# Kernel optimization log

Hardware: AMD Instinct MI355X
Metric: run time of the kernel (lower is better)

The kernel has to match this reference:

```python
import jax, jax.numpy as jnp
import numpy as np

B, T, I = 64, 256, 768   # batch, seq_len (sentences), input_dim
H = 384                  # hidden per direction (hidden_dim // 2)
D = 768                  # hidden_dim (bidirectional concat)


def _gru_dir(x_tbi, w_ih, w_hh, b_ih, b_hh, reverse):
    """Single-direction GRU, PyTorch gate order [r, z, n]. x_tbi: [T,B,in]."""
    gx = jnp.einsum('tbi,gi->tbg', x_tbi, w_ih) + b_ih  # [T,B,3H] input gates

    def step(h, g):
        gh = h @ w_hh.T + b_hh                       # [B,3H]
        r = jax.nn.sigmoid(g[..., :H] + gh[..., :H])
        z = jax.nn.sigmoid(g[..., H:2 * H] + gh[..., H:2 * H])
        n = jnp.tanh(g[..., 2 * H:] + r * gh[..., 2 * H:])
        h_new = (1.0 - z) * n + z * h
        return h_new, h_new

    h0 = jnp.zeros((x_tbi.shape[1], H), x_tbi.dtype)
    _, ys = jax.lax.scan(step, h0, gx, reverse=reverse)  # ys in time order
    return ys


def setup_inputs() -> dict:
    key = jax.random.key(0)
    ks = jax.random.split(key, 24)
    s = 0.05
    inp = {"Sentences": jax.random.normal(ks[0], (B, T, I), dtype=jnp.float32)}
    idx = 1
    for l, in_dim in ((0, I), (1, D)):
        for d in ("f", "b"):
            inp[f"w_ih_l{l}{d}"] = jax.random.normal(ks[idx], (3 * H, in_dim), dtype=jnp.float32) * s; idx += 1
            inp[f"w_hh_l{l}{d}"] = jax.random.normal(ks[idx], (3 * H, H), dtype=jnp.float32) * s; idx += 1
            inp[f"b_ih_l{l}{d}"] = jax.random.normal(ks[idx], (3 * H,), dtype=jnp.float32) * s; idx += 1
            inp[f"b_hh_l{l}{d}"] = jax.random.normal(ks[idx], (3 * H,), dtype=jnp.float32) * s; idx += 1
    inp["fc_w"] = jax.random.normal(ks[idx], (D, D), dtype=jnp.float32) * s; idx += 1
    inp["fc_b"] = jax.random.normal(ks[idx], (D,), dtype=jnp.float32) * s; idx += 1
    inp["upw_w"] = jax.random.normal(ks[idx], (1, D), dtype=jnp.float32) * s; idx += 1
    inp["upw_b"] = jax.random.normal(ks[idx], (1,), dtype=jnp.float32) * s
    return inp


def reference(Sentences,
              w_ih_l0f, w_hh_l0f, b_ih_l0f, b_hh_l0f,
              w_ih_l0b, w_hh_l0b, b_ih_l0b, b_hh_l0b,
              w_ih_l1f, w_hh_l1f, b_ih_l1f, b_hh_l1f,
              w_ih_l1b, w_hh_l1b, b_ih_l1b, b_hh_l1b,
              fc_w, fc_b, upw_w, upw_b):
    x = jnp.transpose(Sentences, (1, 0, 2))  # [T,B,I]
    # layer 0, bidirectional
    hf = _gru_dir(x, w_ih_l0f, w_hh_l0f, b_ih_l0f, b_hh_l0f, reverse=False)
    hb = _gru_dir(x, w_ih_l0b, w_hh_l0b, b_ih_l0b, b_hh_l0b, reverse=True)
    x = jnp.concatenate([hf, hb], axis=-1)  # [T,B,D]
    # layer 1, bidirectional
    hf = _gru_dir(x, w_ih_l1f, w_hh_l1f, b_ih_l1f, b_hh_l1f, reverse=False)
    hb = _gru_dir(x, w_ih_l1b, w_hh_l1b, b_ih_l1b, b_hh_l1b, reverse=True)
    hidden = jnp.transpose(jnp.concatenate([hf, hb], axis=-1), (1, 0, 2))  # [B,T,D]
    # additive attention pooling
    u = jnp.tanh(hidden @ fc_w.T + fc_b)            # [B,T,D]
    logits = u @ upw_w.T + upw_b                    # [B,T,1]
    alpha = jax.nn.softmax(logits, axis=1)          # softmax over sentences
    return jnp.sum(alpha * hidden, axis=-2)         # [B,D]
```

## Files before the change

kernel.cpp:

```cpp
#include <hip/hip_runtime.h>

#define BB   64
#define TT   256
#define II   768
#define HH   384
#define DD   768
#define G3   1152
#define G6   2304

#define TILE 128
#define BK   16

typedef unsigned long long u64t;
typedef __attribute__((ext_vector_type(4))) unsigned int u32x4;

__global__ __launch_bounds__(256) void gemm_gx(
    const float* __restrict__ X, int xmode,
    const float* __restrict__ wf, const float* __restrict__ wb,
    const float* __restrict__ bif, const float* __restrict__ bib,
    float* __restrict__ gx)
{
    __shared__ float As[BK][TILE + 4];
    __shared__ float Bs[BK][TILE + 4];
    const int tid = threadIdx.x;
    const int tx = tid & 15, ty = tid >> 4;
    const int m0 = blockIdx.y * TILE;
    const int n0 = blockIdx.x * TILE;

    float acc[8][8];
#pragma unroll
    for (int i = 0; i < 8; i++)
#pragma unroll
        for (int j = 0; j < 8; j++) acc[i][j] = 0.f;

    for (int k0 = 0; k0 < 768; k0 += BK) {
#pragma unroll
        for (int l = 0; l < 2; l++) {
            int id = tid + l * 256;
            int r  = id >> 2;
            int kq = (id & 3) * 4;
            int m  = m0 + r;
            const float* src;
            if (xmode == 0) {
                int b = m & 63, t = m >> 6;
                src = X + (size_t)b * (TT * II) + (size_t)t * II + k0 + kq;
            } else {
                src = X + (size_t)m * 768 + k0 + kq;
            }
            float4 v = *(const float4*)src;
            As[kq + 0][r] = v.x; As[kq + 1][r] = v.y;
            As[kq + 2][r] = v.z; As[kq + 3][r] = v.w;
        }
#pragma unroll
        for (int l = 0; l < 2; l++) {
            int id = tid + l * 256;
            int r  = id >> 2;
            int kq = (id & 3) * 4;
            int n  = n0 + r;
            const float* wsrc = (n < G3) ? (wf + (size_t)n * 768)
                                         : (wb + (size_t)(n - G3) * 768);
            float4 v = *(const float4*)(wsrc + k0 + kq);
            Bs[kq + 0][r] = v.x; Bs[kq + 1][r] = v.y;
            Bs[kq + 2][r] = v.z; Bs[kq + 3][r] = v.w;
        }
        __syncthreads();
#pragma unroll
        for (int kk = 0; kk < BK; ++kk) {
            float av[8], bv[8];
            *(float4*)&av[0] = *(const float4*)&As[kk][ty * 8];
            *(float4*)&av[4] = *(const float4*)&As[kk][ty * 8 + 4];
            *(float4*)&bv[0] = *(const float4*)&Bs[kk][tx * 8];
            *(float4*)&bv[4] = *(const float4*)&Bs[kk][tx * 8 + 4];
#pragma unroll
            for (int i = 0; i < 8; i++)
#pragma unroll
                for (int j = 0; j < 8; j++)
                    acc[i][j] = fmaf(av[i], bv[j], acc[i][j]);
        }
        __syncthreads();
    }

#pragma unroll
    for (int i = 0; i < 8; i++) {
        int m = m0 + ty * 8 + i;
        int t = m >> 6, b = m & 63;
        float* dst = gx + ((size_t)t * G6 + n0 + tx * 8) * 64 + b;
#pragma unroll
        for (int j = 0; j < 8; j++) {
            int n = n0 + tx * 8 + j;
            float bias = (n < G3) ? bif[n] : bib[n - G3];
            dst[(size_t)j * 64] = acc[i][j] + bias;
        }
    }
}

__global__ __launch_bounds__(256) void recur5(
    const float* __restrict__ gxT,
    const float* __restrict__ whf, const float* __restrict__ whb,
    const float* __restrict__ bhf, const float* __restrict__ bhb,
    u64t* __restrict__ hbuf,
    float* __restrict__ out)
{
    __shared__ float part[2][4][12][64];

    const int bid  = blockIdx.x;
    const int dir  = bid / 96;
    const int c0   = (bid % 96) * 4;
    const int tid  = threadIdx.x;
    const int lane = tid & 63;
    const int w    = __builtin_amdgcn_readfirstlane(tid >> 6);
    const int c    = c0 + w;

    const float* wh = dir ? whb : whf;
    const float* bh = dir ? bhb : bhf;

    const float* wpp[12];
#pragma unroll
    for (int cc = 0; cc < 4; cc++)
#pragma unroll
        for (int g = 0; g < 3; g++)
            wpp[cc * 3 + g] = wh + (size_t)(g * HH + c0 + cc) * HH + w * 96;

    const float bhr = bh[c], bhz = bh[HH + c], bhn = bh[2 * HH + c];

    u64t* hb = hbuf + (size_t)dir * 2 * (192 * 64 * 2);
    const unsigned va0 = (unsigned)(lane * 16);
    const unsigned va1 = va0 + 4096;
    const unsigned va2 = va0 + 8192;

    float hprev = 0.f;

    for (int s = 0; s < TT; s++) {
        const int t = dir ? (TT - 1 - s) : s;
        const u64t* hcur = hb + (size_t)(s & 1) * (192 * 64 * 2);
        u64t*       hnxt = hb + (size_t)((s & 1) ^ 1) * (192 * 64 * 2);
        const unsigned want = (unsigned)s;

        const float* g0 = gxT + ((size_t)t * G6 + dir * G3) * 64;
        float gr = g0[(size_t)(0 * HH + c) * 64 + lane];
        float gz = g0[(size_t)(1 * HH + c) * 64 + lane];
        float gn = g0[(size_t)(2 * HH + c) * 64 + lane];

        float acc[12];
#pragma unroll
        for (int i = 0; i < 12; i++) acc[i] = 0.f;

#pragma unroll 1
        for (int blk = 0; blk < 4; blk++) {
            const u64t* bp = hcur + (size_t)(w * 48 + blk * 12) * 128;
            unsigned long long base = (unsigned long long)bp;
            u32x4 r[12];

            while (true) {
                asm volatile(
                    "global_load_dwordx4 %0, %12, %15 sc0 sc1\n\t"
                    "global_load_dwordx4 %1, %12, %15 offset:1024 sc0 sc1\n\t"
                    "global_load_dwordx4 %2, %12, %15 offset:2048 sc0 sc1\n\t"
                    "global_load_dwordx4 %3, %12, %15 offset:3072 sc0 sc1\n\t"
                    "global_load_dwordx4 %4, %13, %15 sc0 sc1\n\t"
                    "global_load_dwordx4 %5, %13, %15 offset:1024 sc0 sc1\n\t"
                    "global_load_dwordx4 %6, %13, %15 offset:2048 sc0 sc1\n\t"
                    "global_load_dwordx4 %7, %13, %15 offset:3072 sc0 sc1\n\t"
                    "global_load_dwordx4 %8, %14, %15 sc0 sc1\n\t"
                    "global_load_dwordx4 %9, %14, %15 offset:1024 sc0 sc1\n\t"
                    "global_load_dwordx4 %10, %14, %15 offset:2048 sc0 sc1\n\t"
                    "global_load_dwordx4 %11, %14, %15 offset:3072 sc0 sc1\n\t"
                    "s_waitcnt vmcnt(0)"
                    : "=&v"(r[0]), "=&v"(r[1]), "=&v"(r[2]), "=&v"(r[3]),
                      "=&v"(r[4]), "=&v"(r[5]), "=&v"(r[6]), "=&v"(r[7]),
                      "=&v"(r[8]), "=&v"(r[9]), "=&v"(r[10]), "=&v"(r[11])
                    : "v"(va0), "v"(va1), "v"(va2), "s"(base)
                    : "memory");

                bool ok = true;
#pragma unroll
                for (int jj = 0; jj < 12; jj++)
                    ok = ok && (r[jj].y == want) && (r[jj].w == want);
                if (__all(ok)) break;
                __builtin_amdgcn_s_sleep(1);
            }

#pragma unroll
            for (int jj = 0; jj < 12; jj++) {
                float v0 = __uint_as_float(r[jj].x);
                float v1 = __uint_as_float(r[jj].z);
                const int ko = blk * 24 + jj * 2;
#pragma unroll
                for (int cg = 0; cg < 12; cg++) {
                    acc[cg] = fmaf(v0, wpp[cg][ko],     acc[cg]);
                    acc[cg] = fmaf(v1, wpp[cg][ko + 1], acc[cg]);
                }
            }
        }

#pragma unroll
        for (int cg = 0; cg < 12; cg++)
            part[s & 1][w][cg][lane] = acc[cg];
        __syncthreads();

        const int d0 = w * 3;
        float ar = part[s & 1][0][d0 + 0][lane] + part[s & 1][1][d0 + 0][lane]
                 + part[s & 1][2][d0 + 0][lane] + part[s & 1][3][d0 + 0][lane];
        float az = part[s & 1][0][d0 + 1][lane] + part[s & 1][1][d0 + 1][lane]
                 + part[s & 1][2][d0 + 1][lane] + part[s & 1][3][d0 + 1][lane];
        float an = part[s & 1][0][d0 + 2][lane] + part[s & 1][1][d0 + 2][lane]
                 + part[s & 1][2][d0 + 2][lane] + part[s & 1][3][d0 + 2][lane];

        float ghr = ar + bhr, ghz = az + bhz, ghn = an + bhn;
        float rr  = 1.f / (1.f + expf(-(gr + ghr)));
        float zz  = 1.f / (1.f + expf(-(gz + ghz)));
        float nn  = tanhf(gn + rr * ghn);
        float hnew = (1.f - zz) * nn + zz * hprev;
        hprev = hnew;

        u64t pv = ((u64t)(unsigned)(s + 1) << 32) | (u64t)__float_as_uint(hnew);
        __hip_atomic_store(hnxt + (size_t)(c >> 1) * 128 + lane * 2 + (c & 1),
                           pv, __ATOMIC_RELAXED, __HIP_MEMORY_SCOPE_AGENT);
        out[(size_t)t * (BB * DD) + (size_t)lane * DD + dir * HH + c] = hnew;
    }
}

__global__ __launch_bounds__(256) void attn_logits(
    const float* __restrict__ Xh,
    const float* __restrict__ fcw,
    const float* __restrict__ fcb, const float* __restrict__ upw,
    float* __restrict__ logits)
{
    __shared__ float As[BK][TILE + 4];
    __shared__ float Bs[BK][TILE + 4];
    __shared__ float red[TILE][17];
    const int tid = threadIdx.x;
    const int tx = tid & 15, ty = tid >> 4;
    const int m0 = blockIdx.y * TILE;
    const int n0 = blockIdx.x * TILE;

    float acc[8][8];
#pragma unroll
    for (int i = 0; i < 8; i++)
#pragma unroll
        for (int j = 0; j < 8; j++) acc[i][j] = 0.f;

    for (int k0 = 0; k0 < 768; k0 += BK) {
#pragma unroll
        for (int l = 0; l < 2; l++) {
            int id = tid + l * 256;
            int r  = id >> 2;
            int kq = (id & 3) * 4;
            float4 v = *(const float4*)(Xh + (size_t)(m0 + r) * 768 + k0 + kq);
            As[kq + 0][r] = v.x; As[kq + 1][r] = v.y;
            As[kq + 2][r] = v.z; As[kq + 3][r] = v.w;
        }
#pragma unroll
        for (int l = 0; l < 2; l++) {
            int id = tid + l * 256;
            int r  = id >> 2;
            int kq = (id & 3) * 4;
            float4 v = *(const float4*)(fcw + (size_t)(n0 + r) * 768 + k0 + kq);
            Bs[kq + 0][r] = v.x; Bs[kq + 1][r] = v.y;
            Bs[kq + 2][r] = v.z; Bs[kq + 3][r] = v.w;
        }
        __syncthreads();
#pragma unroll
        for (int kk = 0; kk < BK; ++kk) {
            float av[8], bv[8];
            *(float4*)&av[0] = *(const float4*)&As[kk][ty * 8];
            *(float4*)&av[4] = *(const float4*)&As[kk][ty * 8 + 4];
            *(float4*)&bv[0] = *(const float4*)&Bs[kk][tx * 8];
            *(float4*)&bv[4] = *(const float4*)&Bs[kk][tx * 8 + 4];
#pragma unroll
            for (int i = 0; i < 8; i++)
#pragma unroll
                for (int j = 0; j < 8; j++)
                    acc[i][j] = fmaf(av[i], bv[j], acc[i][j]);
        }
        __syncthreads();
    }

#pragma unroll
    for (int i = 0; i < 8; i++) {
        float p = 0.f;
#pragma unroll
        for (int jj = 0; jj < 8; jj++) {
            int n = n0 + tx * 8 + jj;
            p += tanhf(acc[i][jj] + fcb[n]) * upw[n];
        }
        red[ty * 8 + i][tx] = p;
    }
    __syncthreads();
    if (tid < TILE) {
        float s = 0.f;
#pragma unroll
        for (int x = 0; x < 16; x++) s += red[tid][x];
        int m = m0 + tid;
        int t = m >> 6, b = m & 63;
        atomicAdd(&logits[(size_t)b * TT + t], s);
    }
}

__global__ __launch_bounds__(256) void softmax_pool(
    const float* __restrict__ logits, const float* __restrict__ upwb,
    const float* __restrict__ hidden, float* __restrict__ out)
{
    const int b = blockIdx.x, tid = threadIdx.x;
    __shared__ float sa[256];
    __shared__ float red[256];

    float l = logits[(size_t)b * TT + tid] + upwb[0];
    red[tid] = l; __syncthreads();
    for (int s = 128; s > 0; s >>= 1) {
        if (tid < s) red[tid] = fmaxf(red[tid], red[tid + s]);
        __syncthreads();
    }
    float mx = red[0];
    __syncthreads();
    float e = expf(l - mx);
    sa[tid] = e; red[tid] = e; __syncthreads();
    for (int s = 128; s > 0; s >>= 1) {
        if (tid < s) red[tid] += red[tid + s];
        __syncthreads();
    }
    float inv = 1.f / red[0];

    float o0 = 0.f, o1 = 0.f, o2 = 0.f;
    for (int t = 0; t < TT; t++) {
        float a = sa[t] * inv;
        const float* hp = hidden + (size_t)t * (BB * DD) + (size_t)b * DD;
        o0 = fmaf(a, hp[tid],       o0);
        o1 = fmaf(a, hp[tid + 256], o1);
        o2 = fmaf(a, hp[tid + 512], o2);
    }
    out[(size_t)b * DD + tid]       = o0;
    out[(size_t)b * DD + tid + 256] = o1;
    out[(size_t)b * DD + tid + 512] = o2;
}

extern "C" void kernel_launch(void* const* d_in, const int* in_sizes, int n_in,
                              void* d_out, int out_size, void* d_ws, size_t ws_size,
                              hipStream_t stream)
{
    const float* S        = (const float*)d_in[0];
    const float* w_ih_l0f = (const float*)d_in[1];
    const float* w_hh_l0f = (const float*)d_in[2];
    const float* b_ih_l0f = (const float*)d_in[3];
    const float* b_hh_l0f = (const float*)d_in[4];
    const float* w_ih_l0b = (const float*)d_in[5];
    const float* w_hh_l0b = (const float*)d_in[6];
    const float* b_ih_l0b = (const float*)d_in[7];
    const float* b_hh_l0b = (const float*)d_in[8];
    const float* w_ih_l1f = (const float*)d_in[9];
    const float* w_hh_l1f = (const float*)d_in[10];
    const float* b_ih_l1f = (const float*)d_in[11];
    const float* b_hh_l1f = (const float*)d_in[12];
    const float* w_ih_l1b = (const float*)d_in[13];
    const float* w_hh_l1b = (const float*)d_in[14];
    const float* b_ih_l1b = (const float*)d_in[15];
    const float* b_hh_l1b = (const float*)d_in[16];
    const float* fc_w     = (const float*)d_in[17];
    const float* fc_b     = (const float*)d_in[18];
    const float* upw_w    = (const float*)d_in[19];
    const float* upw_b    = (const float*)d_in[20];

    float* gxT    = (float*)d_ws;
    float* buf2   = gxT  + (size_t)TT * G6 * BB;
    float* hbuf   = buf2 + (size_t)TT * BB * DD;
    float* logits = hbuf + (size_t)196608;

    hipMemsetAsync(hbuf, 0, (size_t)(196608 + 16384) * sizeof(float), stream);

    gemm_gx<<<dim3(18, 128), 256, 0, stream>>>(S, 0, w_ih_l0f, w_ih_l0b,
                                               b_ih_l0f, b_ih_l0b, gxT);
    {
        u64t* hb = (u64t*)hbuf;
        void* args[] = {(void*)&gxT, (void*)&w_hh_l0f, (void*)&w_hh_l0b,
                        (void*)&b_hh_l0f, (void*)&b_hh_l0b, (void*)&hb,
                        (void*)&buf2};
        hipLaunchCooperativeKernel((const void*)recur5, dim3(192), dim3(256),
                                   args, 0, stream);
    }
    hipMemsetAsync(hbuf, 0, (size_t)196608 * sizeof(float), stream);

    gemm_gx<<<dim3(18, 128), 256, 0, stream>>>(buf2, 1, w_ih_l1f, w_ih_l1b,
                                               b_ih_l1f, b_ih_l1b, gxT);
    {
        u64t* hb = (u64t*)hbuf;
        void* args[] = {(void*)&gxT, (void*)&w_hh_l1f, (void*)&w_hh_l1b,
                        (void*)&b_hh_l1f, (void*)&b_hh_l1b, (void*)&hb,
                        (void*)&buf2};
        hipLaunchCooperativeKernel((const void*)recur5, dim3(192), dim3(256),
                                   args, 0, stream);
    }
    attn_logits<<<dim3(6, 128), 256, 0, stream>>>(buf2, fc_w, fc_b, upw_w, logits);
    softmax_pool<<<64, 256, 0, stream>>>(logits, upw_b, buf2, (float*)d_out);
}
```

Baseline: 6.381 ms.

## Replace per-value tagged hidden-state polling with separate flag array and packed values

The recurrent kernel previously packed each hidden value with a step tag into 64-bit words and spun re-reading all of them until every tag matched. Now hidden values are stored as plain floats in a k4-interleaved layout, and each column publishes a separate step flag after a waitcnt. Consumers poll only the 384 flags, then read the values once. This halves the bytes read per step and shrinks the polled set. In exchange it adds a store-then-flag ordering that relies on relaxed atomics plus s_waitcnt, which is a memory-ordering risk.

Result: slower. 10.00 ms (+56.7%).

```diff
diff --git a/kernel.cpp b/kernel.cpp
--- a/kernel.cpp
+++ b/kernel.cpp
@@ -12,7 +12,6 @@
 #define BK   16
 
 typedef unsigned long long u64t;
-typedef __attribute__((ext_vector_type(4))) unsigned int u32x4;
 
 __global__ __launch_bounds__(256) void gemm_gx(
     const float* __restrict__ X, int xmode,
@@ -94,18 +93,20 @@
     }
 }
 
-__global__ __launch_bounds__(256) void recur5(
+__global__ __launch_bounds__(256) void recur7(
     const float* __restrict__ gxT,
     const float* __restrict__ whf, const float* __restrict__ whb,
     const float* __restrict__ bhf, const float* __restrict__ bhb,
-    u64t* __restrict__ hbuf,
+    float* __restrict__ hv,
+    unsigned* __restrict__ hf,
     float* __restrict__ out)
 {
     __shared__ float part[2][4][12][64];
 
     const int bid  = blockIdx.x;
     const int dir  = bid / 96;
-    const int c0   = (bid % 96) * 4;
+    const int k4g  = bid % 96;
+    const int c0   = k4g * 4;
     const int tid  = threadIdx.x;
     const int lane = tid & 63;
     const int w    = __builtin_amdgcn_readfirstlane(tid >> 6);
@@ -123,88 +124,72 @@
 
     const float bhr = bh[c], bhz = bh[HH + c], bhn = bh[2 * HH + c];
 
-    u64t* hb = hbuf + (size_t)dir * 2 * (192 * 64 * 2);
-    const unsigned va0 = (unsigned)(lane * 16);
-    const unsigned va1 = va0 + 4096;
-    const unsigned va2 = va0 + 8192;
+    float*    hv0 = hv + (size_t)dir * 2 * 24576;
+    unsigned* hf0 = hf + (size_t)dir * 2 * 384;
 
     float hprev = 0.f;
 
     for (int s = 0; s < TT; s++) {
-        const int t = dir ? (TT - 1 - s) : s;
-        const u64t* hcur = hb + (size_t)(s & 1) * (192 * 64 * 2);
-        u64t*       hnxt = hb + (size_t)((s & 1) ^ 1) * (192 * 64 * 2);
-        const unsigned want = (unsigned)s;
-
-        const float* g0 = gxT + ((size_t)t * G6 + dir * G3) * 64;
-        float gr = g0[(size_t)(0 * HH + c) * 64 + lane];
-        float gz = g0[(size_t)(1 * HH + c) * 64 + lane];
-        float gn = g0[(size_t)(2 * HH + c) * 64 + lane];
+        const int t  = dir ? (TT - 1 - s) : s;
+        const int pp = s & 1;
+        const float*    hvp = hv0 + (size_t)pp * 24576;
+        const unsigned* hfp = hf0 + (size_t)pp * 384;
+        const unsigned  want = (unsigned)s;
+
+        const float* gp = gxT + ((size_t)t * G6 + dir * G3 + c) * 64 + lane;
+        float gr = gp[0];
+        float gz = gp[(size_t)HH * 64];
+        float gn = gp[(size_t)2 * HH * 64];
+
+        while (true) {
+            unsigned f0 = __hip_atomic_load(hfp + lane,       __ATOMIC_RELAXED, __HIP_MEMORY_SCOPE_AGENT);
+            unsigned f1 = __hip_atomic_load(hfp + lane + 64,  __ATOMIC_RELAXED, __HIP_MEMORY_SCOPE_AGENT);
+            unsigned f2 = __hip_atomic_load(hfp + lane + 128, __ATOMIC_RELAXED, __HIP_MEMORY_SCOPE_AGENT);
+            unsigned f3 = __hip_atomic_load(hfp + lane + 192, __ATOMIC_RELAXED, __HIP_MEMORY_SCOPE_AGENT);
+            unsigned f4 = __hip_atomic_load(hfp + lane + 256, __ATOMIC_RELAXED, __HIP_MEMORY_SCOPE_AGENT);
+            unsigned f5 = __hip_atomic_load(hfp + lane + 320, __ATOMIC_RELAXED, __HIP_MEMORY_SCOPE_AGENT);
+            bool ok = (f0 >= want) && (f1 >= want) && (f2 >= want) &&
+                      (f3 >= want) && (f4 >= want) && (f5 >= want);
+            if (__all(ok)) break;
+            __builtin_amdgcn_s_sleep(1);
+        }
 
         float acc[12];
 #pragma unroll
         for (int i = 0; i < 12; i++) acc[i] = 0.f;
 
-#pragma unroll 1
-        for (int blk = 0; blk < 4; blk++) {
-            const u64t* bp = hcur + (size_t)(w * 48 + blk * 12) * 128;
-            unsigned long long base = (unsigned long long)bp;
-            u32x4 r[12];
-
-            while (true) {
-                asm volatile(
-                    "global_load_dwordx4 %0, %12, %15 sc0 sc1\n\t"
-                    "global_load_dwordx4 %1, %12, %15 offset:1024 sc0 sc1\n\t"
-                    "global_load_dwordx4 %2, %12, %15 offset:2048 sc0 sc1\n\t"
-                    "global_load_dwordx4 %3, %12, %15 offset:3072 sc0 sc1\n\t"
-                    "global_load_dwordx4 %4, %13, %15 sc0 sc1\n\t"
-                    "global_load_dwordx4 %5, %13, %15 offset:1024 sc0 sc1\n\t"
-                    "global_load_dwordx4 %6, %13, %15 offset:2048 sc0 sc1\n\t"
-                    "global_load_dwordx4 %7, %13, %15 offset:3072 sc0 sc1\n\t"
-                    "global_load_dwordx4 %8, %14, %15 sc0 sc1\n\t"
-                    "global_load_dwordx4 %9, %14, %15 offset:1024 sc0 sc1\n\t"
-                    "global_load_dwordx4 %10, %14, %15 offset:2048 sc0 sc1\n\t"
-                    "global_load_dwordx4 %11, %14, %15 offset:3072 sc0 sc1\n\t"
-                    "s_waitcnt vmcnt(0)"
-                    : "=&v"(r[0]), "=&v"(r[1]), "=&v"(r[2]), "=&v"(r[3]),
-                      "=&v"(r[4]), "=&v"(r[5]), "=&v"(r[6]), "=&v"(r[7]),
-                      "=&v"(r[8]), "=&v"(r[9]), "=&v"(r[10]), "=&v"(r[11])
-                    : "v"(va0), "v"(va1), "v"(va2), "s"(base)
-                    : "memory");
-
-                bool ok = true;
-#pragma unroll
-                for (int jj = 0; jj < 12; jj++)
-                    ok = ok && (r[jj].y == want) && (r[jj].w == want);
-                if (__all(ok)) break;
-                __builtin_amdgcn_s_sleep(1);
+        const u64t* hv64 = (const u64t*)hvp;
+#pragma unroll
+        for (int g = 0; g < 24; g++) {
+            const size_t off = (size_t)(w * 24 + g) * 128 + lane * 2;
+            u64t p0 = __hip_atomic_load(hv64 + off,     __ATOMIC_RELAXED, __HIP_MEMORY_SCOPE_AGENT);
+            u64t p1 = __hip_atomic_load(hv64 + off + 1, __ATOMIC_RELAXED, __HIP_MEMORY_SCOPE_AGENT);
+            float v0 = __uint_as_float((unsigned)p0);
+            float v1 = __uint_as_float((unsigned)(p0 >> 32));
+            float v2 = __uint_as_float((unsigned)p1);
+            float v3 = __uint_as_float((unsigned)(p1 >> 32));
+#pragma unroll
+            for (int cg = 0; cg < 12; cg++) {
+                const float* wrow = wpp[cg] + g * 4;
+                acc[cg] = fmaf(v0, wrow[0], acc[cg]);
+                acc[cg] = fmaf(v1, wrow[1], acc[cg]);
+                acc[cg] = fmaf(v2, wrow[2], acc[cg]);
+                acc[cg] = fmaf(v3, wrow[3], acc[cg]);
             }
-
-#pragma unroll
-            for (int jj = 0; jj < 12; jj++) {
-                float v0 = __uint_as_float(r[jj].x);
-                float v1 = __uint_as_float(r[jj].z);
-                const int ko = blk * 24 + jj * 2;
-#pragma unroll
-                for (int cg = 0; cg < 12; cg++) {
-                    acc[cg] = fmaf(v0, wpp[cg][ko],     acc[cg]);
-                    acc[cg] = fmaf(v1, wpp[cg][ko + 1], acc[cg]);
-                }
-            }
         }
 
 #pragma unroll
         for (int cg = 0; cg < 12; cg++)
-            part[s & 1][w][cg][lane] = acc[cg];
+            part[pp][w][cg][lane] = acc[cg];
         __syncthreads();
 
         const int d0 = w * 3;
-        float ar = part[s & 1][0][d0 + 0][lane] + part[s & 1][1][d0 + 0][lane]
-                 + part[s & 1][2][d0 + 0][lane] + part[s & 1][3][d0 + 0][lane];
-        float az = part[s & 1][0][d0 + 1][lane] + part[s & 1][1][d0 + 1][lane]
-                 + part[s & 1][2][d0 + 1][lane] + part[s & 1][3][d0 + 1][lane];
-        float an = part[s & 1][0][d0 + 2][lane] + part[s & 1][1][d0 + 2][lane]
-                 + part[s & 1][2][d0 + 2][lane] + part[s & 1][3][d0 + 2][lane];
+        float ar = part[pp][0][d0 + 0][lane] + part[pp][1][d0 + 0][lane]
+                 + part[pp][2][d0 + 0][lane] + part[pp][3][d0 + 0][lane];
+        float az = part[pp][0][d0 + 1][lane] + part[pp][1][d0 + 1][lane]
+                 + part[pp][2][d0 + 1][lane] + part[pp][3][d0 + 1][lane];
+        float an = part[pp][0][d0 + 2][lane] + part[pp][1][d0 + 2][lane]
+                 + part[pp][2][d0 + 2][lane] + part[pp][3][d0 + 2][lane];
 
         float ghr = ar + bhr, ghz = az + bhz, ghn = an + bhn;
         float rr  = 1.f / (1.f + expf(-(gr + ghr)));
@@ -213,9 +198,17 @@
         float hnew = (1.f - zz) * nn + zz * hprev;
         hprev = hnew;
 
-        u64t pv = ((u64t)(unsigned)(s + 1) << 32) | (u64t)__float_as_uint(hnew);
-        __hip_atomic_store(hnxt + (size_t)(c >> 1) * 128 + lane * 2 + (c & 1),
-                           pv, __ATOMIC_RELAXED, __HIP_MEMORY_SCOPE_AGENT);
+        {
+            float* hvn = hv0 + (size_t)(pp ^ 1) * 24576;
+            __hip_atomic_store(hvn + (size_t)k4g * 256 + lane * 4 + w, hnew,
+                               __ATOMIC_RELAXED, __HIP_MEMORY_SCOPE_AGENT);
+            asm volatile("s_waitcnt vmcnt(0)" ::: "memory");
+            if (lane == 0) {
+                unsigned* hfn = hf0 + (size_t)(pp ^ 1) * 384;
+                __hip_atomic_store(hfn + c, (unsigned)(s + 1),
+                                   __ATOMIC_RELAXED, __HIP_MEMORY_SCOPE_AGENT);
+            }
+        }
         out[(size_t)t * (BB * DD) + (size_t)lane * DD + dir * HH + c] = hnew;
     }
 }
@@ -360,33 +353,32 @@
     const float* upw_w    = (const float*)d_in[19];
     const float* upw_b    = (const float*)d_in[20];
 
-    float* gxT    = (float*)d_ws;
-    float* buf2   = gxT  + (size_t)TT * G6 * BB;
-    float* hbuf   = buf2 + (size_t)TT * BB * DD;
-    float* logits = hbuf + (size_t)196608;
-
-    hipMemsetAsync(hbuf, 0, (size_t)(196608 + 16384) * sizeof(float), stream);
+    float* gxT     = (float*)d_ws;
+    float* buf2    = gxT  + (size_t)TT * G6 * BB;
+    float* hv      = buf2 + (size_t)TT * BB * DD;
+    unsigned* hfl  = (unsigned*)(hv + 98304);
+    float* logits  = (float*)(hfl + 1536);
+
+    hipMemsetAsync(hv, 0, (size_t)(98304 + 1536 + 16384) * 4, stream);
 
     gemm_gx<<<dim3(18, 128), 256, 0, stream>>>(S, 0, w_ih_l0f, w_ih_l0b,
                                                b_ih_l0f, b_ih_l0b, gxT);
     {
-        u64t* hb = (u64t*)hbuf;
         void* args[] = {(void*)&gxT, (void*)&w_hh_l0f, (void*)&w_hh_l0b,
-                        (void*)&b_hh_l0f, (void*)&b_hh_l0b, (void*)&hb,
-                        (void*)&buf2};
-        hipLaunchCooperativeKernel((const void*)recur5, dim3(192), dim3(256),
+                        (void*)&b_hh_l0f, (void*)&b_hh_l0b, (void*)&hv,
+                        (void*)&hfl, (void*)&buf2};
+        hipLaunchCooperativeKernel((const void*)recur7, dim3(192), dim3(256),
                                    args, 0, stream);
     }
-    hipMemsetAsync(hbuf, 0, (size_t)196608 * sizeof(float), stream);
+    hipMemsetAsync(hv, 0, (size_t)(98304 + 1536) * 4, stream);
 
     gemm_gx<<<dim3(18, 128), 256, 0, stream>>>(buf2, 1, w_ih_l1f, w_ih_l1b,
                                                b_ih_l1f, b_ih_l1b, gxT);
     {
-        u64t* hb = (u64t*)hbuf;
         void* args[] = {(void*)&gxT, (void*)&w_hh_l1f, (void*)&w_hh_l1b,
-                        (void*)&b_hh_l1f, (void*)&b_hh_l1b, (void*)&hb,
-                        (void*)&buf2};
-        hipLaunchCooperativeKernel((const void*)recur5, dim3(192), dim3(256),
+                        (void*)&b_hh_l1f, (void*)&b_hh_l1b, (void*)&hv,
+                        (void*)&hfl, (void*)&buf2};
+        hipLaunchCooperativeKernel((const void*)recur7, dim3(192), dim3(256),
                                    args, 0, stream);
     }
     attn_logits<<<dim3(6, 128), 256, 0, stream>>>(buf2, fc_w, fc_b, upw_w, logits);
```
